# Optimization experiments

Measured on AMD Instinct MI355X. Metric: run time of the kernel, lower is better.

## Reference

```python
import jax, jax.numpy as jnp
import numpy as np

B, L, D = 1, 2048, 2048
H, KV, HD = 32, 8, 64
REP = H // KV  # GQA repeat factor = 4


def _rope(t, cos, sin):
    # t: (B, L, nH, HD); cos/sin: (L, HD//2). Complex rotation on (even, odd) pairs.
    tr = t.reshape(*t.shape[:-1], HD // 2, 2)
    xr, xi = tr[..., 0], tr[..., 1]
    c = cos[None, :, None, :]
    s = sin[None, :, None, :]
    out_r = xr * c - xi * s
    out_i = xr * s + xi * c
    return jnp.stack([out_r, out_i], axis=-1).reshape(t.shape)


def setup_inputs() -> dict:
    key = jax.random.key(0)
    ks = jax.random.split(key, 5)
    x = jax.random.normal(ks[0], (B, L, D), jnp.float32)
    wq = jax.random.normal(ks[1], (D, H * HD), jnp.float32) * 0.02
    wk = jax.random.normal(ks[2], (D, KV * HD), jnp.float32) * 0.02
    wv = jax.random.normal(ks[3], (D, KV * HD), jnp.float32) * 0.02
    wo = jax.random.normal(ks[4], (H * HD, D), jnp.float32) * 0.02
    pos = jnp.arange(L, dtype=jnp.float32)
    inv_freq = 1.0 / (10000.0 ** (jnp.arange(0, HD, 2, dtype=jnp.float32) / HD))
    ang = pos[:, None] * inv_freq[None, :]  # (L, HD//2)
    freqs_cos = jnp.cos(ang)
    freqs_sin = jnp.sin(ang)
    # causal additive mask (L, L): 0 on/below diagonal, large negative above
    causal = jnp.arange(L)[None, :] <= jnp.arange(L)[:, None]
    mask = jnp.where(causal, 0.0, -1e9).astype(jnp.float32)
    return {"x": x, "wq": wq, "wk": wk, "wv": wv, "wo": wo,
            "freqs_cos": freqs_cos, "freqs_sin": freqs_sin, "mask": mask}


def reference(x, wq, wk, wv, wo, freqs_cos, freqs_sin, mask):
    q = (x @ wq).reshape(B, L, H, HD)
    k = (x @ wk).reshape(B, L, KV, HD)
    v = (x @ wv).reshape(B, L, KV, HD)
    q = _rope(q, freqs_cos, freqs_sin)
    k = _rope(k, freqs_cos, freqs_sin)
    # GQA: repeat_interleave kv heads
    k = jnp.repeat(k, REP, axis=2)
    v = jnp.repeat(v, REP, axis=2)
    # (B, nH, L, HD)
    q = q.transpose(0, 2, 1, 3)
    k = k.transpose(0, 2, 1, 3)
    v = v.transpose(0, 2, 1, 3)
    scores = jnp.einsum('bhqd,bhkd->bhqk', q, k) / np.float32(np.sqrt(HD))
    scores = scores + mask[None, None, :, :]
    attn = jax.nn.softmax(scores.astype(jnp.float32), axis=-1).astype(q.dtype)
    out = jnp.einsum('bhqk,bhkd->bqhd', attn, v).reshape(B, L, H * HD)
    return out @ wo
```

## Files before the change

### kernel.cpp

```cpp
#include <hip/hip_runtime.h>
#include <hip/hip_bf16.h>

#define L 2048
#define D 2048
#define NH 32
#define NKV 8
#define HD 64

typedef unsigned short u16;
typedef __attribute__((ext_vector_type(8))) short bf16x8;
typedef __attribute__((ext_vector_type(4))) short bf16x4;
typedef __attribute__((ext_vector_type(4))) float f32x4;

#define QSCALE 0.1803368801f

__device__ __forceinline__ f32x4 mfma16(bf16x4 a, bf16x4 b, f32x4 c) {
    return __builtin_amdgcn_mfma_f32_16x16x16bf16_1k(a, b, c, 0, 0, 0);
}

#define PANEL_OFF(d0, k) ((((size_t)((d0) >> 7) * 64 + ((k) >> 5)) << 12) + (((d0) & 127) << 5) + ((k) & 31))

__device__ __forceinline__ u16 f2bf(float x) {
    __hip_bfloat16 b = __float2bfloat16(x);
    return *reinterpret_cast<u16*>(&b);
}

__device__ __forceinline__ void gload_lds16(const void* g, void* l) {
    __builtin_amdgcn_global_load_lds(
        (const __attribute__((address_space(1))) unsigned int*)g,
        (__attribute__((address_space(3))) unsigned int*)l, 16, 0, 0);
}

__global__ __launch_bounds__(256) void prep_kernel(
    const float* __restrict__ x, u16* __restrict__ xb,
    const float* __restrict__ wq, const float* __restrict__ wk,
    const float* __restrict__ wv, const float* __restrict__ wo,
    u16* __restrict__ wqkvT, u16* __restrict__ woT)
{
    const int z = blockIdx.z;
    if (z == 4) {
        int i = (blockIdx.y * 64 + blockIdx.x) * 256 + threadIdx.x;
        int e = i * 4;
        int row = e >> 11, k0 = e & 2047;
        float4 v = ((const float4*)x)[i];
        ushort4 o;
        o.x = f2bf(v.x); o.y = f2bf(v.y); o.z = f2bf(v.z); o.w = f2bf(v.w);
        *(ushort4*)&xb[PANEL_OFF(row, k0)] = o;
        return;
    }
    const float* src; u16* dst; int C;
    if (z == 0)      { src = wq; dst = wqkvT;                           C = 2048; }
    else if (z == 1) { src = wk; dst = wqkvT + (size_t)2048 * 2048;     C = 512;  }
    else if (z == 2) { src = wv; dst = wqkvT + (size_t)2560 * 2048;     C = 512;  }
    else             { src = wo; dst = woT;                             C = 2048; }
    const int c0 = blockIdx.x * 32;
    if (c0 >= C) return;
    const int r0 = blockIdx.y * 32;
    __shared__ float tile[32][33];
    const int tx = threadIdx.x & 31, ty = threadIdx.x >> 5;
#pragma unroll
    for (int i = 0; i < 32; i += 8)
        tile[ty + i][tx] = src[(size_t)(r0 + ty + i) * C + c0 + tx];
    __syncthreads();
#pragma unroll
    for (int i = 0; i < 32; i += 8) {
        const int n = c0 + ty + i, k = r0 + tx;
        dst[PANEL_OFF(n, k)] = f2bf(tile[tx][ty + i]);
    }
}

#define VT_LDS 72

template <int MODE>
__global__ __launch_bounds__(256) void gemm4w_kernel(
    const u16* __restrict__ A, const u16* __restrict__ Bt, void* __restrict__ Cout,
    int N, int K, const float* __restrict__ fc, const float* __restrict__ fs,
    u16* __restrict__ vt)
{
    __shared__ __align__(16) u16 As[4][128 * 32];
    __shared__ __align__(16) u16 Bs[4][128 * 32];
    const int tid = threadIdx.x;
    const int w = tid >> 6, lane = tid & 63;

    const int nwg = (int)(gridDim.x * gridDim.y);
    int bid = (int)blockIdx.y * (int)gridDim.x + (int)blockIdx.x;
    bid = (bid & 7) * (nwg >> 3) + (bid >> 3);
    const int m0 = (bid / (int)gridDim.x) * 128, n0 = (bid % (int)gridDim.x) * 128;

    const int l15 = lane & 15, quad = lane >> 4, q8 = quad * 8;
    const int wr = (w >> 1) * 64, wc = (w & 1) * 64;
    const int l8 = lane * 8;
    const int wch = w * 1024;

    const u16* pa = A  + ((size_t)(m0 >> 7) * (K / 32) << 12);
    const u16* pb = Bt + ((size_t)(n0 >> 7) * (K / 32) << 12);

    f32x4 acc[4][4];
#pragma unroll
    for (int i = 0; i < 4; ++i)
#pragma unroll
        for (int j = 0; j < 4; ++j) acc[i][j] = (f32x4){0.f, 0.f, 0.f, 0.f};

    const int nSub = K / 32;
    const int nOut = nSub / 2;
#pragma unroll
    for (int s = 0; s < 4; ++s) {
        const size_t so = (size_t)s << 12;
        gload_lds16(pa + so + wch + l8,       &As[s][wch]);
        gload_lds16(pa + so + wch + 512 + l8, &As[s][wch + 512]);
        gload_lds16(pb + so + wch + l8,       &Bs[s][wch]);
        gload_lds16(pb + so + wch + 512 + l8, &Bs[s][wch + 512]);
    }
    for (int it = 0; it < nOut; ++it) {
        const int s0 = 2 * it, cb0 = s0 & 3, cb1 = (s0 + 1) & 3;
        asm volatile("s_waitcnt vmcnt(8)" ::: "memory");
        asm volatile("s_barrier" ::: "memory");
        bf16x8 a0[4], a1[4], b0[4], b1[4];
#pragma unroll
        for (int t = 0; t < 4; ++t) {
            a0[t] = *(const bf16x8*)&As[cb0][(wr + t * 16 + l15) * 32 + q8];
            b0[t] = *(const bf16x8*)&Bs[cb0][(wc + t * 16 + l15) * 32 + q8];
            a1[t] = *(const bf16x8*)&As[cb1][(wr + t * 16 + l15) * 32 + q8];
            b1[t] = *(const bf16x8*)&Bs[cb1][(wc + t * 16 + l15) * 32 + q8];
        }
        asm volatile("s_waitcnt lgkmcnt(0)" ::: "memory");
        asm volatile("s_barrier" ::: "memory");
        {
            const int sp0 = s0 + 4, sp1 = s0 + 5;
            const size_t k0 = (size_t)((sp0 < nSub) ? sp0 : 0) << 12;
            const size_t k1 = (size_t)((sp1 < nSub) ? sp1 : 0) << 12;
            gload_lds16(pa + k0 + wch + l8,       &As[cb0][wch]);
            gload_lds16(pa + k0 + wch + 512 + l8, &As[cb0][wch + 512]);
            gload_lds16(pb + k0 + wch + l8,       &Bs[cb0][wch]);
            gload_lds16(pb + k0 + wch + 512 + l8, &Bs[cb0][wch + 512]);
            gload_lds16(pa + k1 + wch + l8,       &As[cb1][wch]);
            gload_lds16(pa + k1 + wch + 512 + l8, &As[cb1][wch + 512]);
            gload_lds16(pb + k1 + wch + l8,       &Bs[cb1][wch]);
            gload_lds16(pb + k1 + wch + 512 + l8, &Bs[cb1][wch + 512]);
        }
#pragma unroll
        for (int i = 0; i < 4; ++i)
#pragma unroll
            for (int j = 0; j < 4; ++j) {
                acc[i][j] = __builtin_amdgcn_mfma_f32_16x16x32_bf16(a0[i], b0[j], acc[i][j], 0, 0, 0);
                acc[i][j] = __builtin_amdgcn_mfma_f32_16x16x32_bf16(a1[i], b1[j], acc[i][j], 0, 0, 0);
            }
    }

    if (MODE == 0) {
        float* C = (float*)Cout;
#pragma unroll
        for (int i = 0; i < 4; ++i)
#pragma unroll
            for (int j = 0; j < 4; ++j)
#pragma unroll
                for (int r = 0; r < 4; ++r)
                    C[(size_t)(m0 + wr + i * 16 + quad * 4 + r) * N + n0 + wc + j * 16 + l15] = acc[i][j][r];
    } else {
        __syncthreads();
        u16* O = (u16*)Cout;
        const int vc0 = n0 + wc;
        if (vc0 < 2560) {
            const float scl = (vc0 < 2048) ? QSCALE : 1.0f;
            const int odd = l15 & 1;
#pragma unroll
            for (int i = 0; i < 4; ++i)
#pragma unroll
                for (int j = 0; j < 4; ++j)
#pragma unroll
                    for (int r = 0; r < 4; ++r) {
                        const int row = m0 + wr + i * 16 + quad * 4 + r;
                        const int col = vc0 + j * 16 + l15;
                        float v = acc[i][j][r];
                        const int i2 = (j * 16 + l15) >> 1;
                        const float c = fc[row * 32 + i2], s = fs[row * 32 + i2];
                        const float p = __shfl_xor(v, 1);
                        float o = (odd ? (p * s + v * c) : (v * c - p * s)) * scl;
                        O[(size_t)row * 3072 + col] = f2bf(o);
                    }
        } else {
            u16* ws_ = (w < 2 ? (u16*)As : (u16*)Bs) + (w & 1) * (64 * VT_LDS);
#pragma unroll
            for (int i = 0; i < 4; ++i)
#pragma unroll
                for (int j = 0; j < 4; ++j)
#pragma unroll
                    for (int r = 0; r < 4; ++r)
                        ws_[(j * 16 + l15) * VT_LDS + i * 16 + quad * 4 + r] = f2bf(acc[i][j][r]);
#pragma unroll
            for (int t = 0; t < 8; ++t) {
                const int vr = t * 8 + (lane >> 3);
                const int c8 = (lane & 7) * 8;
                bf16x8 vv = *(const bf16x8*)&ws_[vr * VT_LDS + c8];
                *(bf16x8*)&vt[(size_t)(vc0 - 2560 + vr) * 2048 + m0 + wr + c8] = vv;
            }
        }
    }
}

__global__ __launch_bounds__(256) void attn_mfma_kernel(
    const u16* __restrict__ qkv,
    const u16* __restrict__ vt,
    u16* __restrict__ ab)
{
    __shared__ __align__(16) u16 Ks[2][64 * 64];
    __shared__ __align__(16) u16 Vs[2][64 * 64];

    const int h = blockIdx.x;
    const int tile = (int)gridDim.y - 1 - (int)blockIdx.y;
    const int gkv = h >> 2;
    const int tid = threadIdx.x;
    const int w = tid >> 6, lane = tid & 63;
    const int l15 = lane & 15, quad = lane >> 4;
    const int q0 = tile * 64 + w * 16;

    const int srow = lane >> 3, schunk = lane & 7;
    const int r0_ = w * 16 + srow, r1_ = w * 16 + 8 + srow;
    const int c0_ = (schunk ^ (r0_ & 7)) * 8, c1_ = (schunk ^ (r1_ & 7)) * 8;
    const u16* kbase = qkv + 2048 + gkv * HD;
    const u16* vbase = vt + (size_t)gkv * HD * 2048;

    bf16x8 qa[2];
    {
        const u16* qrow = qkv + (size_t)(q0 + l15) * 3072 + h * HD + quad * 8;
        qa[0] = *(const bf16x8*)(qrow);
        qa[1] = *(const bf16x8*)(qrow + 32);
    }
    f32x4 O[4];
#pragma unroll
    for (int i = 0; i < 4; ++i) O[i] = (f32x4){0.f, 0.f, 0.f, 0.f};
    float m_run = -1e30f;
    float l_run = 0.f;

    gload_lds16(kbase + (size_t)r0_ * 3072 + c0_, &Ks[0][(w * 16) * 64]);
    gload_lds16(kbase + (size_t)r1_ * 3072 + c1_, &Ks[0][(w * 16 + 8) * 64]);
    gload_lds16(vbase + (size_t)r0_ * 2048 + c0_, &Vs[0][(w * 16) * 64]);
    gload_lds16(vbase + (size_t)r1_ * 2048 + c1_, &Vs[0][(w * 16 + 8) * 64]);

    for (int c = 0; c <= tile; ++c) {
        const int cb = c & 1, nb = cb ^ 1;
        const int kn = (c < tile ? c + 1 : tile) * 64;
        gload_lds16(kbase + (size_t)(kn + r0_) * 3072 + c0_, &Ks[nb][(w * 16) * 64]);
        gload_lds16(kbase + (size_t)(kn + r1_) * 3072 + c1_, &Ks[nb][(w * 16 + 8) * 64]);
        gload_lds16(vbase + (size_t)r0_ * 2048 + kn + c0_,   &Vs[nb][(w * 16) * 64]);
        gload_lds16(vbase + (size_t)r1_ * 2048 + kn + c1_,   &Vs[nb][(w * 16 + 8) * 64]);
        asm volatile("s_waitcnt vmcnt(4)" ::: "memory");
        asm volatile("s_barrier" ::: "memory");

        f32x4 s[4];
        __builtin_amdgcn_s_setprio(1);
#pragma unroll
        for (int kt = 0; kt < 4; ++kt) {
            const int kr = kt * 16 + l15, kx = (kr & 7);
            bf16x8 b0 = *(const bf16x8*)&Ks[cb][kr * 64 + ((quad ^ kx) * 8)];
            bf16x8 b1 = *(const bf16x8*)&Ks[cb][kr * 64 + (((quad + 4) ^ kx) * 8)];
            f32x4 t = (f32x4){0.f, 0.f, 0.f, 0.f};
            t = __builtin_amdgcn_mfma_f32_16x16x32_bf16(b0, qa[0], t, 0, 0, 0);
            t = __builtin_amdgcn_mfma_f32_16x16x32_bf16(b1, qa[1], t, 0, 0, 0);
            s[kt] = t;
        }
        __builtin_amdgcn_s_setprio(0);
        if (c == tile) {
#pragma unroll
            for (int kt = 0; kt < 4; ++kt)
#pragma unroll
                for (int r = 0; r < 4; ++r)
                    if (kt * 16 + quad * 4 + r > w * 16 + l15) s[kt][r] = -1e30f;
        }
        float mx = fmaxf(fmaxf(fmaxf(s[0][0], s[0][1]), fmaxf(s[0][2], s[0][3])),
                         fmaxf(fmaxf(s[1][0], s[1][1]), fmaxf(s[1][2], s[1][3])));
        mx = fmaxf(mx, fmaxf(fmaxf(fmaxf(s[2][0], s[2][1]), fmaxf(s[2][2], s[2][3])),
                             fmaxf(fmaxf(s[3][0], s[3][1]), fmaxf(s[3][2], s[3][3]))));
        mx = fmaxf(mx, __shfl_xor(mx, 16));
        mx = fmaxf(mx, __shfl_xor(mx, 32));
        const bool resc = !__all(mx <= m_run + 8.f);
        float aL = 1.f;
        if (resc) {
            const float mn = fmaxf(m_run, mx);
            aL = exp2f(m_run - mn);
            m_run = mn;
        }
#pragma unroll
        for (int kt = 0; kt < 4; ++kt)
#pragma unroll
            for (int r = 0; r < 4; ++r) s[kt][r] = exp2f(s[kt][r] - m_run);
        float rsum = 0.f;
#pragma unroll
        for (int kt = 0; kt < 4; ++kt)
#pragma unroll
            for (int r = 0; r < 4; ++r) rsum += s[kt][r];
        rsum += __shfl_xor(rsum, 16);
        rsum += __shfl_xor(rsum, 32);
        l_run = resc ? (l_run * aL + rsum) : (l_run + rsum);
        bf16x4 pbf[4];
#pragma unroll
        for (int kt = 0; kt < 4; ++kt) {
            unsigned int lo, hi;
            asm("v_cvt_pk_bf16_f32 %0, %1, %2" : "=v"(lo) : "v"(s[kt][0]), "v"(s[kt][1]));
            asm("v_cvt_pk_bf16_f32 %0, %1, %2" : "=v"(hi) : "v"(s[kt][2]), "v"(s[kt][3]));
            union { unsigned int u[2]; bf16x4 v; } cv;
            cv.u[0] = lo; cv.u[1] = hi;
            pbf[kt] = cv.v;
        }
        if (resc) {
#pragma unroll
            for (int r = 0; r < 4; ++r) {
                const float aQ = __shfl(aL, (quad << 4) + (quad << 2) + r);
                O[0][r] *= aQ; O[1][r] *= aQ; O[2][r] *= aQ; O[3][r] *= aQ;
            }
        }
        __builtin_amdgcn_s_setprio(1);
#pragma unroll
        for (int dt = 0; dt < 4; ++dt) {
            const int vr = dt * 16 + l15, vx = (vr & 7);
#pragma unroll
            for (int kt = 0; kt < 4; ++kt) {
                bf16x4 vf = *(const bf16x4*)&Vs[cb][vr * 64 +
                    (((2 * kt + (quad >> 1)) ^ vx) << 3) + ((quad & 1) << 2)];
                O[dt] = mfma16(pbf[kt], vf, O[dt]);
            }
        }
        __builtin_amdgcn_s_setprio(0);
        asm volatile("s_barrier" ::: "memory");
    }
#pragma unroll
    for (int r = 0; r < 4; ++r) {
        const float lq = __shfl(l_run, (quad << 4) + (quad << 2) + r);
        const float inv = 1.0f / lq;
        const int q = q0 + quad * 4 + r;
        const int pbase = ((q >> 7) << 18) + ((q & 127) << 5);
#pragma unroll
        for (int dt = 0; dt < 4; ++dt) {
            const int col = h * HD + dt * 16 + l15;
            ab[pbase + ((col >> 5) << 12) + (col & 31)] = f2bf(O[dt][r] * inv);
        }
    }
}

extern "C" void kernel_launch(void* const* d_in, const int* in_sizes, int n_in,
                              void* d_out, int out_size, void* d_ws, size_t ws_size,
                              hipStream_t stream)
{
    const float* x  = (const float*)d_in[0];
    const float* wq = (const float*)d_in[1];
    const float* wk = (const float*)d_in[2];
    const float* wv = (const float*)d_in[3];
    const float* wo = (const float*)d_in[4];
    const float* fc = (const float*)d_in[5];
    const float* fs = (const float*)d_in[6];
    float* out = (float*)d_out;

    u16* xb     = (u16*)d_ws;
    u16* wqkvT  = xb     + (size_t)2048 * 2048;
    u16* woT    = wqkvT  + (size_t)3072 * 2048;
    u16* qkv_bf = woT    + (size_t)2048 * 2048;
    u16* vt     = qkv_bf + (size_t)2048 * 3072;
    u16* ab     = vt     + (size_t)512 * 2048;

    prep_kernel<<<dim3(64, 64, 5), 256, 0, stream>>>(x, xb, wq, wk, wv, wo, wqkvT, woT);

    gemm4w_kernel<1><<<dim3(3072 / 128, 2048 / 128), 256, 0, stream>>>(
        xb, wqkvT, qkv_bf, 3072, 2048, fc, fs, vt);

    attn_mfma_kernel<<<dim3(NH, L / 64), 256, 0, stream>>>(qkv_bf, vt, ab);

    gemm4w_kernel<0><<<dim3(2048 / 128, 2048 / 128), 256, 0, stream>>>(
        ab, woT, out, 2048, 2048, nullptr, nullptr, nullptr);
}
```

Before: 245.3 us.

## Share KV tiles across GQA heads, pair causal tiles, widen prep transpose tiles

The attention kernel now assigns one KV group per block, with each of the four waves handling one of the four query heads that share that group. Each K/V tile loaded into LDS is therefore reused by four heads. Each block processes two 32-row query tiles (p and 63-p) back to back to balance causal work, cutting the grid to 8x32 blocks. The prep kernel separately switches to 64x64 transpose tiles with float4 loads and 16-byte bf16 stores, and the x conversion handles four vectors per thread. The trade-offs are fewer, longer-running blocks (lower occupancy and parallelism) and more complex pointer resets between the two tiles.

New measurement: 283.7 us. 1.16x slower.

```diff
diff --git a/kernel.cpp b/kernel.cpp
--- a/kernel.cpp
+++ b/kernel.cpp
@@ -38,14 +38,19 @@
     u16* __restrict__ wqkvT, u16* __restrict__ woT)
 {
     const int z = blockIdx.z;
+    const int tid = threadIdx.x;
     if (z == 4) {
-        int i = (blockIdx.y * 64 + blockIdx.x) * 256 + threadIdx.x;
-        int e = i * 4;
-        int row = e >> 11, k0 = e & 2047;
-        float4 v = ((const float4*)x)[i];
-        ushort4 o;
-        o.x = f2bf(v.x); o.y = f2bf(v.y); o.z = f2bf(v.z); o.w = f2bf(v.w);
-        *(ushort4*)&xb[PANEL_OFF(row, k0)] = o;
+        const int base = (blockIdx.y * 32 + blockIdx.x) * 1024 + tid;
+#pragma unroll
+        for (int k = 0; k < 4; ++k) {
+            const int i = base + k * 256;
+            const int e = i * 4;
+            const int row = e >> 11, k0 = e & 2047;
+            float4 v = ((const float4*)x)[i];
+            ushort4 o;
+            o.x = f2bf(v.x); o.y = f2bf(v.y); o.z = f2bf(v.z); o.w = f2bf(v.w);
+            *(ushort4*)&xb[PANEL_OFF(row, k0)] = o;
+        }
         return;
     }
     const float* src; u16* dst; int C;
@@ -53,19 +58,29 @@
     else if (z == 1) { src = wk; dst = wqkvT + (size_t)2048 * 2048;     C = 512;  }
     else if (z == 2) { src = wv; dst = wqkvT + (size_t)2560 * 2048;     C = 512;  }
     else             { src = wo; dst = woT;                             C = 2048; }
-    const int c0 = blockIdx.x * 32;
+    const int c0 = blockIdx.x * 64;
     if (c0 >= C) return;
-    const int r0 = blockIdx.y * 32;
-    __shared__ float tile[32][33];
-    const int tx = threadIdx.x & 31, ty = threadIdx.x >> 5;
-#pragma unroll
-    for (int i = 0; i < 32; i += 8)
-        tile[ty + i][tx] = src[(size_t)(r0 + ty + i) * C + c0 + tx];
+    const int r0 = blockIdx.y * 64;
+    __shared__ float tile[64][65];
+    {
+        const int b4 = (tid & 15) * 4, ty = tid >> 4;
+#pragma unroll
+        for (int i = 0; i < 4; ++i) {
+            const int a = ty + i * 16;
+            float4 v = *(const float4*)&src[(size_t)(r0 + a) * C + c0 + b4];
+            tile[a][b4] = v.x; tile[a][b4 + 1] = v.y;
+            tile[a][b4 + 2] = v.z; tile[a][b4 + 3] = v.w;
+        }
+    }
     __syncthreads();
-#pragma unroll
-    for (int i = 0; i < 32; i += 8) {
-        const int n = c0 + ty + i, k = r0 + tx;
-        dst[PANEL_OFF(n, k)] = f2bf(tile[tx][ty + i]);
+    {
+        const int j = tid & 63, h16 = (tid >> 6) * 16;
+        u16 buf[16];
+#pragma unroll
+        for (int t = 0; t < 16; ++t) buf[t] = f2bf(tile[h16 + t][j]);
+        u16* d = &dst[PANEL_OFF(c0 + j, r0 + h16)];
+        *(bf16x8*)d       = *(bf16x8*)&buf[0];
+        *(bf16x8*)(d + 8) = *(bf16x8*)&buf[8];
     }
 }
 
@@ -198,6 +213,31 @@
     }
 }
 
+#define LOAD_Q(T)                                                              \
+    {                                                                          \
+        const u16* q0p = qkv + (size_t)((T) * 32 + l15) * 3072 + h * HD + quad * 8; \
+        qa[0][0] = *(const bf16x8*)(q0p);                                      \
+        qa[0][1] = *(const bf16x8*)(q0p + 32);                                 \
+        qa[1][0] = *(const bf16x8*)(q0p + 16 * 3072);                          \
+        qa[1][1] = *(const bf16x8*)(q0p + 16 * 3072 + 32);                     \
+    }
+
+#define EPILOGUE(T)                                                            \
+    _Pragma("unroll")                                                          \
+    for (int sub = 0; sub < 2; ++sub)                                          \
+        _Pragma("unroll")                                                      \
+        for (int r = 0; r < 4; ++r) {                                          \
+            const float lq = __shfl(l_run[sub], (quad << 4) + (quad << 2) + r);\
+            const float inv = 1.0f / lq;                                       \
+            const int q = (T) * 32 + sub * 16 + quad * 4 + r;                  \
+            const int pbase = ((q >> 7) << 18) + ((q & 127) << 5);             \
+            _Pragma("unroll")                                                  \
+            for (int dt = 0; dt < 4; ++dt) {                                   \
+                const int col = h * HD + dt * 16 + l15;                        \
+                ab[pbase + ((col >> 5) << 12) + (col & 31)] = f2bf(O[sub][dt][r] * inv); \
+            }                                                                  \
+        }
+
 __global__ __launch_bounds__(256) void attn_mfma_kernel(
     const u16* __restrict__ qkv,
     const u16* __restrict__ vt,
@@ -206,135 +246,157 @@
     __shared__ __align__(16) u16 Ks[2][64 * 64];
     __shared__ __align__(16) u16 Vs[2][64 * 64];
 
-    const int h = blockIdx.x;
-    const int tile = (int)gridDim.y - 1 - (int)blockIdx.y;
-    const int gkv = h >> 2;
+    const int gkv = blockIdx.x;
+    const int p   = blockIdx.y;
     const int tid = threadIdx.x;
     const int w = tid >> 6, lane = tid & 63;
     const int l15 = lane & 15, quad = lane >> 4;
-    const int q0 = tile * 64 + w * 16;
+    const int h = gkv * 4 + w;
 
     const int srow = lane >> 3, schunk = lane & 7;
-    const int r0_ = w * 16 + srow, r1_ = w * 16 + 8 + srow;
+    const int r0_ = w * 16 + srow, r1_ = r0_ + 8;
     const int c0_ = (schunk ^ (r0_ & 7)) * 8, c1_ = (schunk ^ (r1_ & 7)) * 8;
-    const u16* kbase = qkv + 2048 + gkv * HD;
-    const u16* vbase = vt + (size_t)gkv * HD * 2048;
-
-    bf16x8 qa[2];
-    {
-        const u16* qrow = qkv + (size_t)(q0 + l15) * 3072 + h * HD + quad * 8;
-        qa[0] = *(const bf16x8*)(qrow);
-        qa[1] = *(const bf16x8*)(qrow + 32);
-    }
-    f32x4 O[4];
-#pragma unroll
-    for (int i = 0; i < 4; ++i) O[i] = (f32x4){0.f, 0.f, 0.f, 0.f};
-    float m_run = -1e30f;
-    float l_run = 0.f;
-
-    gload_lds16(kbase + (size_t)r0_ * 3072 + c0_, &Ks[0][(w * 16) * 64]);
-    gload_lds16(kbase + (size_t)r1_ * 3072 + c1_, &Ks[0][(w * 16 + 8) * 64]);
-    gload_lds16(vbase + (size_t)r0_ * 2048 + c0_, &Vs[0][(w * 16) * 64]);
-    gload_lds16(vbase + (size_t)r1_ * 2048 + c1_, &Vs[0][(w * 16 + 8) * 64]);
-
-    for (int c = 0; c <= tile; ++c) {
-        const int cb = c & 1, nb = cb ^ 1;
-        const int kn = (c < tile ? c + 1 : tile) * 64;
-        gload_lds16(kbase + (size_t)(kn + r0_) * 3072 + c0_, &Ks[nb][(w * 16) * 64]);
-        gload_lds16(kbase + (size_t)(kn + r1_) * 3072 + c1_, &Ks[nb][(w * 16 + 8) * 64]);
-        gload_lds16(vbase + (size_t)r0_ * 2048 + kn + c0_,   &Vs[nb][(w * 16) * 64]);
-        gload_lds16(vbase + (size_t)r1_ * 2048 + kn + c1_,   &Vs[nb][(w * 16 + 8) * 64]);
+    const u16* kb0 = qkv + 2048 + gkv * HD + (size_t)r0_ * 3072 + c0_;
+    const u16* kb1 = qkv + 2048 + gkv * HD + (size_t)r1_ * 3072 + c1_;
+    const u16* vb0 = vt + (size_t)(gkv * HD + r0_) * 2048 + c0_;
+    const u16* vb1 = vt + (size_t)(gkv * HD + r1_) * 2048 + c1_;
+    const u16 *pk0 = kb0, *pk1 = kb1, *pv0 = vb0, *pv1 = vb1;
+
+    const int kx = l15 & 7;
+    const int aK  = l15 * 128 + ((quad ^ kx) * 16);
+    const int aK2 = aK ^ 64;
+    const int aV  = l15 * 128 + (((quad >> 1) ^ kx) * 16) + ((quad & 1) * 8);
+
+    const int tA = p, tB = 63 - p;
+    const int nA = (tA >> 1) + 1;
+    const int ntot = nA + (tB >> 1) + 1;
+
+    bf16x8 qa[2][2];
+    LOAD_Q(tA);
+
+    f32x4 O[2][4];
+#pragma unroll
+    for (int sub = 0; sub < 2; ++sub)
+#pragma unroll
+        for (int i = 0; i < 4; ++i) O[sub][i] = (f32x4){0.f, 0.f, 0.f, 0.f};
+    float m_run[2] = {-1e30f, -1e30f};
+    float l_run[2] = {0.f, 0.f};
+    int qoff = (tA & 1) * 32;
+
+    gload_lds16(pk0, &Ks[0][(w * 16) * 64]);
+    gload_lds16(pk1, &Ks[0][(w * 16 + 8) * 64]);
+    gload_lds16(pv0, &Vs[0][(w * 16) * 64]);
+    gload_lds16(pv1, &Vs[0][(w * 16 + 8) * 64]);
+    pk0 += 64 * 3072; pk1 += 64 * 3072; pv0 += 64; pv1 += 64;
+    if (nA == 1) { pk0 = kb0; pk1 = kb1; pv0 = vb0; pv1 = vb1; }
+
+    for (int s = 0; s < ntot; ++s) {
+        const int cb = s & 1;
+        gload_lds16(pk0, &Ks[cb ^ 1][(w * 16) * 64]);
+        gload_lds16(pk1, &Ks[cb ^ 1][(w * 16 + 8) * 64]);
+        gload_lds16(pv0, &Vs[cb ^ 1][(w * 16) * 64]);
+        gload_lds16(pv1, &Vs[cb ^ 1][(w * 16 + 8) * 64]);
+        pk0 += 64 * 3072; pk1 += 64 * 3072; pv0 += 64; pv1 += 64;
         asm volatile("s_waitcnt vmcnt(4)" ::: "memory");
         asm volatile("s_barrier" ::: "memory");
 
-        f32x4 s[4];
-        __builtin_amdgcn_s_setprio(1);
-#pragma unroll
-        for (int kt = 0; kt < 4; ++kt) {
-            const int kr = kt * 16 + l15, kx = (kr & 7);
-            bf16x8 b0 = *(const bf16x8*)&Ks[cb][kr * 64 + ((quad ^ kx) * 8)];
-            bf16x8 b1 = *(const bf16x8*)&Ks[cb][kr * 64 + (((quad + 4) ^ kx) * 8)];
-            f32x4 t = (f32x4){0.f, 0.f, 0.f, 0.f};
-            t = __builtin_amdgcn_mfma_f32_16x16x32_bf16(b0, qa[0], t, 0, 0, 0);
-            t = __builtin_amdgcn_mfma_f32_16x16x32_bf16(b1, qa[1], t, 0, 0, 0);
-            s[kt] = t;
-        }
-        __builtin_amdgcn_s_setprio(0);
-        if (c == tile) {
+        if (s == nA) {
+            EPILOGUE(tA);
+            LOAD_Q(tB);
+#pragma unroll
+            for (int sub = 0; sub < 2; ++sub) {
+#pragma unroll
+                for (int i = 0; i < 4; ++i) O[sub][i] = (f32x4){0.f, 0.f, 0.f, 0.f};
+                m_run[sub] = -1e30f;
+                l_run[sub] = 0.f;
+            }
+            qoff = (tB & 1) * 32;
+        }
+        const bool diag = (s == nA - 1) || (s == ntot - 1);
+        const char* KB = (const char*)Ks + cb * 8192;
+        const char* VB = (const char*)Vs + cb * 8192;
+
+#pragma unroll
+        for (int sub = 0; sub < 2; ++sub) {
+            f32x4 sv[4];
+            __builtin_amdgcn_s_setprio(1);
+#pragma unroll
+            for (int kt = 0; kt < 4; ++kt) {
+                bf16x8 b0 = *(const bf16x8*)(KB + kt * 2048 + aK);
+                bf16x8 b1 = *(const bf16x8*)(KB + kt * 2048 + aK2);
+                f32x4 t = (f32x4){0.f, 0.f, 0.f, 0.f};
+                t = __builtin_amdgcn_mfma_f32_16x16x32_bf16(b0, qa[sub][0], t, 0, 0, 0);
+                t = __builtin_amdgcn_mfma_f32_16x16x32_bf16(b1, qa[sub][1], t, 0, 0, 0);
+                sv[kt] = t;
+            }
+            __builtin_amdgcn_s_setprio(0);
+            if (diag) {
+                const int qr = qoff + sub * 16 + l15;
+#pragma unroll
+                for (int kt = 0; kt < 4; ++kt)
+#pragma unroll
+                    for (int r = 0; r < 4; ++r)
+                        if (kt * 16 + quad * 4 + r > qr) sv[kt][r] = -1e30f;
+            }
+            float mx = fmaxf(fmaxf(fmaxf(sv[0][0], sv[0][1]), fmaxf(sv[0][2], sv[0][3])),
+                             fmaxf(fmaxf(sv[1][0], sv[1][1]), fmaxf(sv[1][2], sv[1][3])));
+            mx = fmaxf(mx, fmaxf(fmaxf(fmaxf(sv[2][0], sv[2][1]), fmaxf(sv[2][2], sv[2][3])),
+                                 fmaxf(fmaxf(sv[3][0], sv[3][1]), fmaxf(sv[3][2], sv[3][3]))));
+            mx = fmaxf(mx, __shfl_xor(mx, 16));
+            mx = fmaxf(mx, __shfl_xor(mx, 32));
+            const bool resc = !__all(mx <= m_run[sub] + 8.f);
+            float aL = 1.f;
+            if (resc) {
+                const float mn = fmaxf(m_run[sub], mx);
+                aL = exp2f(m_run[sub] - mn);
+                m_run[sub] = mn;
+            }
 #pragma unroll
             for (int kt = 0; kt < 4; ++kt)
 #pragma unroll
-                for (int r = 0; r < 4; ++r)
-                    if (kt * 16 + quad * 4 + r > w * 16 + l15) s[kt][r] = -1e30f;
-        }
-        float mx = fmaxf(fmaxf(fmaxf(s[0][0], s[0][1]), fmaxf(s[0][2], s[0][3])),
-                         fmaxf(fmaxf(s[1][0], s[1][1]), fmaxf(s[1][2], s[1][3])));
-        mx = fmaxf(mx, fmaxf(fmaxf(fmaxf(s[2][0], s[2][1]), fmaxf(s[2][2], s[2][3])),
-                             fmaxf(fmaxf(s[3][0], s[3][1]), fmaxf(s[3][2], s[3][3]))));
-        mx = fmaxf(mx, __shfl_xor(mx, 16));
-        mx = fmaxf(mx, __shfl_xor(mx, 32));
-        const bool resc = !__all(mx <= m_run + 8.f);
-        float aL = 1.f;
-        if (resc) {
-            const float mn = fmaxf(m_run, mx);
-            aL = exp2f(m_run - mn);
-            m_run = mn;
-        }
-#pragma unroll
-        for (int kt = 0; kt < 4; ++kt)
-#pragma unroll
-            for (int r = 0; r < 4; ++r) s[kt][r] = exp2f(s[kt][r] - m_run);
-        float rsum = 0.f;
-#pragma unroll
-        for (int kt = 0; kt < 4; ++kt)
-#pragma unroll
-            for (int r = 0; r < 4; ++r) rsum += s[kt][r];
-        rsum += __shfl_xor(rsum, 16);
-        rsum += __shfl_xor(rsum, 32);
-        l_run = resc ? (l_run * aL + rsum) : (l_run + rsum);
-        bf16x4 pbf[4];
-#pragma unroll
-        for (int kt = 0; kt < 4; ++kt) {
-            unsigned int lo, hi;
-            asm("v_cvt_pk_bf16_f32 %0, %1, %2" : "=v"(lo) : "v"(s[kt][0]), "v"(s[kt][1]));
-            asm("v_cvt_pk_bf16_f32 %0, %1, %2" : "=v"(hi) : "v"(s[kt][2]), "v"(s[kt][3]));
-            union { unsigned int u[2]; bf16x4 v; } cv;
-            cv.u[0] = lo; cv.u[1] = hi;
-            pbf[kt] = cv.v;
-        }
-        if (resc) {
-#pragma unroll
-            for (int r = 0; r < 4; ++r) {
-                const float aQ = __shfl(aL, (quad << 4) + (quad << 2) + r);
-                O[0][r] *= aQ; O[1][r] *= aQ; O[2][r] *= aQ; O[3][r] *= aQ;
-            }
-        }
-        __builtin_amdgcn_s_setprio(1);
-#pragma unroll
-        for (int dt = 0; dt < 4; ++dt) {
-            const int vr = dt * 16 + l15, vx = (vr & 7);
+                for (int r = 0; r < 4; ++r) sv[kt][r] = exp2f(sv[kt][r] - m_run[sub]);
+            float rsum = 0.f;
+#pragma unroll
+            for (int kt = 0; kt < 4; ++kt)
+#pragma unroll
+                for (int r = 0; r < 4; ++r) rsum += sv[kt][r];
+            rsum += __shfl_xor(rsum, 16);
+            rsum += __shfl_xor(rsum, 32);
+            l_run[sub] = resc ? (l_run[sub] * aL + rsum) : (l_run[sub] + rsum);
+            bf16x4 pbf[4];
 #pragma unroll
             for (int kt = 0; kt < 4; ++kt) {
-                bf16x4 vf = *(const bf16x4*)&Vs[cb][vr * 64 +
-                    (((2 * kt + (quad >> 1)) ^ vx) << 3) + ((quad & 1) << 2)];
-                O[dt] = mfma16(pbf[kt], vf, O[dt]);
-            }
-        }
-        __builtin_amdgcn_s_setprio(0);
+                unsigned int lo, hi;
+                asm("v_cvt_pk_bf16_f32 %0, %1, %2" : "=v"(lo) : "v"(sv[kt][0]), "v"(sv[kt][1]));
+                asm("v_cvt_pk_bf16_f32 %0, %1, %2" : "=v"(hi) : "v"(sv[kt][2]), "v"(sv[kt][3]));
+                union { unsigned int u[2]; bf16x4 v; } cv;
+                cv.u[0] = lo; cv.u[1] = hi;
+                pbf[kt] = cv.v;
+            }
+            if (resc) {
+#pragma unroll
+                for (int r = 0; r < 4; ++r) {
+                    const float aQ = __shfl(aL, (quad << 4) + (quad << 2) + r);
+                    O[sub][0][r] *= aQ; O[sub][1][r] *= aQ;
+                    O[sub][2][r] *= aQ; O[sub][3][r] *= aQ;
+                }
+            }
+            __builtin_amdgcn_s_setprio(1);
+#pragma unroll
+            for (int kt = 0; kt < 4; ++kt) {
+                const int aVk = aV ^ (kt * 32);
+#pragma unroll
+                for (int dt = 0; dt < 4; ++dt) {
+                    bf16x4 vf = *(const bf16x4*)(VB + dt * 2048 + aVk);
+                    O[sub][dt] = mfma16(pbf[kt], vf, O[sub][dt]);
+                }
+            }
+            __builtin_amdgcn_s_setprio(0);
+        }
         asm volatile("s_barrier" ::: "memory");
-    }
-#pragma unroll
-    for (int r = 0; r < 4; ++r) {
-        const float lq = __shfl(l_run, (quad << 4) + (quad << 2) + r);
-        const float inv = 1.0f / lq;
-        const int q = q0 + quad * 4 + r;
-        const int pbase = ((q >> 7) << 18) + ((q & 127) << 5);
-#pragma unroll
-        for (int dt = 0; dt < 4; ++dt) {
-            const int col = h * HD + dt * 16 + l15;
-            ab[pbase + ((col >> 5) << 12) + (col & 31)] = f2bf(O[dt][r] * inv);
-        }
-    }
+        if (s == nA - 2) { pk0 = kb0; pk1 = kb1; pv0 = vb0; pv1 = vb1; }
+    }
+    EPILOGUE(tB);
 }
 
 extern "C" void kernel_launch(void* const* d_in, const int* in_sizes, int n_in,
@@ -357,12 +419,12 @@
     u16* vt     = qkv_bf + (size_t)2048 * 3072;
     u16* ab     = vt     + (size_t)512 * 2048;
 
-    prep_kernel<<<dim3(64, 64, 5), 256, 0, stream>>>(x, xb, wq, wk, wv, wo, wqkvT, woT);
+    prep_kernel<<<dim3(32, 32, 5), 256, 0, stream>>>(x, xb, wq, wk, wv, wo, wqkvT, woT);
 
     gemm4w_kernel<1><<<dim3(3072 / 128, 2048 / 128), 256, 0, stream>>>(
         xb, wqkvT, qkv_bf, 3072, 2048, fc, fs, vt);
 
-    attn_mfma_kernel<<<dim3(NH, L / 64), 256, 0, stream>>>(qkv_bf, vt, ab);
+    attn_mfma_kernel<<<dim3(NKV, 32), 256, 0, stream>>>(qkv_bf, vt, ab);
 
     gemm4w_kernel<0><<<dim3(2048 / 128, 2048 / 128), 256, 0, stream>>>(
         ab, woT, out, 2048, 2048, nullptr, nullptr, nullptr);
```
